# Kernel optimization log

Measured on AMD Instinct MI355X. Metric: run time of the kernel, lower is better.

Reference implementation:

```python
import jax, jax.numpy as jnp
import numpy as np


def setup_inputs() -> dict:
    key = jax.random.key(0)
    k1, k2 = jax.random.split(key)
    N, C, H, W = 8, 64, 256, 256
    Ho, Wo = 256, 256
    x = jax.random.normal(k1, (N, C, H, W), dtype=jnp.float32)
    # most values in [-1,1], a few outside to exercise zeros padding
    grid = jax.random.uniform(k2, (N, Ho, Wo, 2), dtype=jnp.float32,
                              minval=-1.1, maxval=1.1)
    return {"x": x, "grid": grid}


def _grid_sample_bilinear_zeros(x, grid):
    # x: [N,C,H,W], grid: [N,Ho,Wo,2] (dx,dy) normalized; align_corners=False
    N, C, H, W = x.shape
    # unnormalize: align_corners=False -> ((g+1)*size - 1) / 2
    ix = ((grid[..., 0] + 1.0) * W - 1.0) * 0.5  # [N,Ho,Wo]
    iy = ((grid[..., 1] + 1.0) * H - 1.0) * 0.5

    x0f = jnp.floor(ix)
    y0f = jnp.floor(iy)
    x0 = x0f.astype(jnp.int32)
    y0 = y0f.astype(jnp.int32)
    x1 = x0 + 1
    y1 = y0 + 1

    # bilinear weights
    tx = ix - x0f  # fractional part
    ty = iy - y0f
    w00 = (1.0 - tx) * (1.0 - ty)
    w01 = tx * (1.0 - ty)
    w10 = (1.0 - tx) * ty
    w11 = tx * ty

    b = jnp.arange(N)[:, None, None]  # broadcast batch index [N,1,1]

    def gather(yi, xi):
        # zeros padding: mask out-of-bounds taps
        valid = ((xi >= 0) & (xi < W) & (yi >= 0) & (yi < H)).astype(x.dtype)
        xc = jnp.clip(xi, 0, W - 1)
        yc = jnp.clip(yi, 0, H - 1)
        v = x[b, :, yc, xc]  # advanced indexing -> [N,Ho,Wo,C]
        return v * valid[..., None]

    out = (gather(y0, x0) * w00[..., None]
           + gather(y0, x1) * w01[..., None]
           + gather(y1, x0) * w10[..., None]
           + gather(y1, x1) * w11[..., None])  # [N,Ho,Wo,C]
    return jnp.transpose(out, (0, 3, 1, 2))  # [N,C,Ho,Wo]


def reference(x, grid):
    out = _grid_sample_bilinear_zeros(x, grid)
    return out.astype(x.dtype)
```

## Files before the change

### kernel.cpp

```cpp
#include <hip/hip_runtime.h>
#include <hip/hip_bf16.h>


#define GS_N 8
#define GS_C 64
#define GS_H 256
#define GS_W 256
#define GS_HW (GS_H * GS_W)
#define GS_PIX (GS_N * GS_HW)

__device__ __forceinline__ float bf_lo(unsigned u) { return __uint_as_float(u << 16); }
__device__ __forceinline__ float bf_hi(unsigned u) { return __uint_as_float(u & 0xFFFF0000u); }

__device__ __forceinline__ unsigned pack_bf16x2(float lo, float hi) {
    unsigned ul = __float_as_uint(lo);
    unsigned uh = __float_as_uint(hi);
    ul = (ul + 0x7FFFu + ((ul >> 16) & 1u)) >> 16;
    uh = (uh + 0x7FFFu + ((uh >> 16) & 1u)) & 0xFFFF0000u;
    return ul | uh;
}

__global__ __launch_bounds__(256) void transpose_tasks_bf16(
    const float* __restrict__ x, unsigned* __restrict__ xt32)
{
    __shared__ float tile[32][132];

    const int t = threadIdx.x;
    const int k = blockIdx.x & 7;
    const int j = blockIdx.x >> 3;
    const int task = k + ((j >= 512) ? 8 : 0);
    const int within = j & 511;
    const int n = task >> 1;
    const int h = task & 1;
    const int hw_base = within << 7;

    {
        const int c_l = t >> 5;
        const int px4 = (t & 31) << 2;
        const float* __restrict__ xb = x + ((size_t)n << 22) + ((size_t)(h * 32) << 16);
#pragma unroll
        for (int i = 0; i < 4; ++i) {
            const int c = c_l + (i << 3);
            const float4 v = *(const float4*)(xb + (size_t)c * GS_HW + hw_base + px4);
            *(float4*)&tile[c][px4] = v;
        }
    }
    __syncthreads();
    {
        const int pih = t & 15;
        const int hwq = t >> 4;
        const size_t tbase = ((size_t)task << 16) + hw_base;
#pragma unroll
        for (int i = 0; i < 8; ++i) {
            const int hw = hwq + (i << 4);
            const unsigned v = pack_bf16x2(tile[2 * pih][hw], tile[2 * pih + 1][hw]);
            xt32[((tbase + hw) << 4) + pih] = v;
        }
    }
}

__global__ __launch_bounds__(256) void sample_tasks_bf16(
    const unsigned* __restrict__ xt32,
    const float* __restrict__ grid,
    float* __restrict__ out)
{
    const int t = threadIdx.x;
    const int k = blockIdx.x & 7;
    const int j = blockIdx.x >> 3;
    const int task = k + ((j < 512) ? 8 : 0);
    const int within = j & 511;
    const int n = task >> 1;
    const int half = task & 1;

    const int p_local = (t & 63) | ((t & 128) >> 1);
    const int sub = (t >> 6) & 1;

    const int hwp = (within << 7) + p_local;
    const int pix = (n << 16) + hwp;

    const float gx = grid[pix * 2 + 0];
    const float gy = grid[pix * 2 + 1];

    const float ix = ((gx + 1.0f) * (float)GS_W - 1.0f) * 0.5f;
    const float iy = ((gy + 1.0f) * (float)GS_H - 1.0f) * 0.5f;

    const float x0f = floorf(ix);
    const float y0f = floorf(iy);
    const int x0 = (int)x0f, y0 = (int)y0f;
    const int x1 = x0 + 1,   y1 = y0 + 1;

    const float tx = ix - x0f;
    const float ty = iy - y0f;

    float w00 = (1.0f - tx) * (1.0f - ty);
    float w01 = tx * (1.0f - ty);
    float w10 = (1.0f - tx) * ty;
    float w11 = tx * ty;

    const bool vx0 = (x0 >= 0) & (x0 < GS_W);
    const bool vx1 = (x1 >= 0) & (x1 < GS_W);
    const bool vy0 = (y0 >= 0) & (y0 < GS_H);
    const bool vy1 = (y1 >= 0) & (y1 < GS_H);
    w00 = (vy0 && vx0) ? w00 : 0.0f;
    w01 = (vy0 && vx1) ? w01 : 0.0f;
    w10 = (vy1 && vx0) ? w10 : 0.0f;
    w11 = (vy1 && vx1) ? w11 : 0.0f;

    const int x0c = min(max(x0, 0), GS_W - 1);
    const int x1c = min(max(x1, 0), GS_W - 1);
    const int y0c = min(max(y0, 0), GS_H - 1);
    const int y1c = min(max(y1, 0), GS_H - 1);

    const size_t tbase = (size_t)task << 16;
    const int sub8 = sub << 3;

    const uint4* __restrict__ p00 = (const uint4*)(xt32 + (((tbase + (size_t)(y0c * GS_W + x0c)) << 4) + sub8));
    const uint4* __restrict__ p01 = (const uint4*)(xt32 + (((tbase + (size_t)(y0c * GS_W + x1c)) << 4) + sub8));
    const uint4* __restrict__ p10 = (const uint4*)(xt32 + (((tbase + (size_t)(y1c * GS_W + x0c)) << 4) + sub8));
    const uint4* __restrict__ p11 = (const uint4*)(xt32 + (((tbase + (size_t)(y1c * GS_W + x1c)) << 4) + sub8));

    const uint4 a0 = p00[0], a1 = p00[1];
    const uint4 b0 = p01[0], b1 = p01[1];
    const uint4 c0 = p10[0], c1 = p10[1];
    const uint4 d0 = p11[0], d1 = p11[1];

    float r[16];
    {
        const unsigned aw[8] = { a0.x, a0.y, a0.z, a0.w, a1.x, a1.y, a1.z, a1.w };
        const unsigned bw[8] = { b0.x, b0.y, b0.z, b0.w, b1.x, b1.y, b1.z, b1.w };
        const unsigned cw[8] = { c0.x, c0.y, c0.z, c0.w, c1.x, c1.y, c1.z, c1.w };
        const unsigned dw[8] = { d0.x, d0.y, d0.z, d0.w, d1.x, d1.y, d1.z, d1.w };
#pragma unroll
        for (int q = 0; q < 8; ++q) {
            float lo = w00 * bf_lo(aw[q]);
            lo = fmaf(w01, bf_lo(bw[q]), lo);
            lo = fmaf(w10, bf_lo(cw[q]), lo);
            lo = fmaf(w11, bf_lo(dw[q]), lo);
            float hi = w00 * bf_hi(aw[q]);
            hi = fmaf(w01, bf_hi(bw[q]), hi);
            hi = fmaf(w10, bf_hi(cw[q]), hi);
            hi = fmaf(w11, bf_hi(dw[q]), hi);
            r[2 * q]     = lo;
            r[2 * q + 1] = hi;
        }
    }

    float* __restrict__ ob = out + ((size_t)n << 22) + ((size_t)(half * 32 + sub * 16) << 16) + hwp;
#pragma unroll
    for (int i = 0; i < 16; ++i) {
        ob[(size_t)i << 16] = r[i];
    }
}

__global__ __launch_bounds__(256) void gridsample_direct(
    const float* __restrict__ x,
    const float* __restrict__ grid,
    float* __restrict__ out)
{
    const int pix = blockIdx.x * blockDim.x + threadIdx.x;
    const int n  = pix >> 16;
    const int hw = pix & 0xFFFF;

    const float gx = grid[pix * 2 + 0];
    const float gy = grid[pix * 2 + 1];
    const float ix = ((gx + 1.0f) * (float)GS_W - 1.0f) * 0.5f;
    const float iy = ((gy + 1.0f) * (float)GS_H - 1.0f) * 0.5f;
    const float x0f = floorf(ix), y0f = floorf(iy);
    const int x0 = (int)x0f, y0 = (int)y0f, x1 = x0 + 1, y1 = y0 + 1;
    const float tx = ix - x0f, ty = iy - y0f;
    float w00 = (1.0f - tx) * (1.0f - ty);
    float w01 = tx * (1.0f - ty);
    float w10 = (1.0f - tx) * ty;
    float w11 = tx * ty;
    const bool vx0 = (x0 >= 0) & (x0 < GS_W);
    const bool vx1 = (x1 >= 0) & (x1 < GS_W);
    const bool vy0 = (y0 >= 0) & (y0 < GS_H);
    const bool vy1 = (y1 >= 0) & (y1 < GS_H);
    w00 = (vy0 && vx0) ? w00 : 0.0f;
    w01 = (vy0 && vx1) ? w01 : 0.0f;
    w10 = (vy1 && vx0) ? w10 : 0.0f;
    w11 = (vy1 && vx1) ? w11 : 0.0f;
    const int x0c = min(max(x0, 0), GS_W - 1);
    const int x1c = min(max(x1, 0), GS_W - 1);
    const int y0c = min(max(y0, 0), GS_H - 1);
    const int y1c = min(max(y1, 0), GS_H - 1);
    const int o00 = y0c * GS_W + x0c;
    const int o01 = y0c * GS_W + x1c;
    const int o10 = y1c * GS_W + x0c;
    const int o11 = y1c * GS_W + x1c;
    const float* __restrict__ xb = x + (size_t)n * GS_C * GS_HW;
    float* __restrict__ ob = out + (size_t)n * GS_C * GS_HW + hw;
#pragma unroll 4
    for (int c = 0; c < GS_C; ++c) {
        const float* __restrict__ xp = xb + (size_t)c * GS_HW;
        float v = w00 * xp[o00];
        v = fmaf(w01, xp[o01], v);
        v = fmaf(w10, xp[o10], v);
        v = fmaf(w11, xp[o11], v);
        ob[(size_t)c * GS_HW] = v;
    }
}

extern "C" void kernel_launch(void* const* d_in, const int* in_sizes, int n_in,
                              void* d_out, int out_size, void* d_ws, size_t ws_size,
                              hipStream_t stream) {
    const float* x    = (const float*)d_in[0];
    const float* grid = (const float*)d_in[1];
    float* out        = (float*)d_out;

    const size_t xt_bytes = (size_t)GS_PIX * GS_C * sizeof(unsigned short);

    if (ws_size >= xt_bytes) {
        unsigned* xt32 = (unsigned*)d_ws;
        transpose_tasks_bf16<<<8192, 256, 0, stream>>>(x, xt32);
        sample_tasks_bf16<<<8192, 256, 0, stream>>>(xt32, grid, out);
    } else {
        gridsample_direct<<<GS_PIX / 256, 256, 0, stream>>>(x, grid, out);
    }
}
```

Baseline: 100.1 us.

## Split transpose/sample into two task halves and use nontemporal loads/stores

Replaces the two full-size launches with four half-size launches, each pair transposing and then sampling 8 tasks (4 batches), so the bf16 workspace for a half can stay in the last-level cache before it is sampled. The x reads, grid reads and output writes now use nontemporal builtins, so streaming traffic is less likely to evict the reused workspace. The cost is two extra kernel launches and less parallelism per launch.

```diff
diff --git a/kernel.cpp b/kernel.cpp
--- a/kernel.cpp
+++ b/kernel.cpp
@@ -9,6 +9,9 @@
 #define GS_HW (GS_H * GS_W)
 #define GS_PIX (GS_N * GS_HW)
 
+typedef float  fx4 __attribute__((ext_vector_type(4)));
+typedef float  fx2 __attribute__((ext_vector_type(2)));
+
 __device__ __forceinline__ float bf_lo(unsigned u) { return __uint_as_float(u << 16); }
 __device__ __forceinline__ float bf_hi(unsigned u) { return __uint_as_float(u & 0xFFFF0000u); }
 
@@ -21,15 +24,14 @@
 }
 
 __global__ __launch_bounds__(256) void transpose_tasks_bf16(
-    const float* __restrict__ x, unsigned* __restrict__ xt32)
+    const float* __restrict__ x, unsigned* __restrict__ xt32, int task_base)
 {
     __shared__ float tile[32][132];
 
     const int t = threadIdx.x;
     const int k = blockIdx.x & 7;
-    const int j = blockIdx.x >> 3;
-    const int task = k + ((j >= 512) ? 8 : 0);
-    const int within = j & 511;
+    const int within = blockIdx.x >> 3;
+    const int task = task_base + k;
     const int n = task >> 1;
     const int h = task & 1;
     const int hw_base = within << 7;
@@ -41,8 +43,9 @@
 #pragma unroll
         for (int i = 0; i < 4; ++i) {
             const int c = c_l + (i << 3);
-            const float4 v = *(const float4*)(xb + (size_t)c * GS_HW + hw_base + px4);
-            *(float4*)&tile[c][px4] = v;
+            const fx4 v = __builtin_nontemporal_load(
+                (const fx4*)(xb + (size_t)c * GS_HW + hw_base + px4));
+            *(fx4*)&tile[c][px4] = v;
         }
     }
     __syncthreads();
@@ -62,13 +65,12 @@
 __global__ __launch_bounds__(256) void sample_tasks_bf16(
     const unsigned* __restrict__ xt32,
     const float* __restrict__ grid,
-    float* __restrict__ out)
+    float* __restrict__ out, int task_base)
 {
     const int t = threadIdx.x;
     const int k = blockIdx.x & 7;
-    const int j = blockIdx.x >> 3;
-    const int task = k + ((j < 512) ? 8 : 0);
-    const int within = j & 511;
+    const int within = blockIdx.x >> 3;
+    const int task = task_base + k;
     const int n = task >> 1;
     const int half = task & 1;
 
@@ -78,8 +80,9 @@
     const int hwp = (within << 7) + p_local;
     const int pix = (n << 16) + hwp;
 
-    const float gx = grid[pix * 2 + 0];
-    const float gy = grid[pix * 2 + 1];
+    const fx2 g = __builtin_nontemporal_load((const fx2*)(grid + (size_t)pix * 2));
+    const float gx = g.x;
+    const float gy = g.y;
 
     const float ix = ((gx + 1.0f) * (float)GS_W - 1.0f) * 0.5f;
     const float iy = ((gy + 1.0f) * (float)GS_H - 1.0f) * 0.5f;
@@ -148,7 +151,7 @@
     float* __restrict__ ob = out + ((size_t)n << 22) + ((size_t)(half * 32 + sub * 16) << 16) + hwp;
 #pragma unroll
     for (int i = 0; i < 16; ++i) {
-        ob[(size_t)i << 16] = r[i];
+        __builtin_nontemporal_store(r[i], ob + ((size_t)i << 16));
     }
 }
 
@@ -212,8 +215,10 @@
 
     if (ws_size >= xt_bytes) {
         unsigned* xt32 = (unsigned*)d_ws;
-        transpose_tasks_bf16<<<8192, 256, 0, stream>>>(x, xt32);
-        sample_tasks_bf16<<<8192, 256, 0, stream>>>(xt32, grid, out);
+        transpose_tasks_bf16<<<4096, 256, 0, stream>>>(x, xt32, 0);
+        sample_tasks_bf16<<<4096, 256, 0, stream>>>(xt32, grid, out, 0);
+        transpose_tasks_bf16<<<4096, 256, 0, stream>>>(x, xt32, 8);
+        sample_tasks_bf16<<<4096, 256, 0, stream>>>(xt32, grid, out, 8);
     } else {
         gridsample_direct<<<GS_PIX / 256, 256, 0, stream>>>(x, grid, out);
     }
```

Measured after the change: 108.8 us. 8.7% more time.
